# Optimization experiments

Hardware: AMD Instinct MI355X
Metric: run time of the kernel (lower is better)

The kernel has to match this reference:

```python
import jax, jax.numpy as jnp
import numpy as np

N_NODES = 100000
N_EDGES = 3200000
DIM = 64


def setup_inputs() -> dict:
    key = jax.random.key(0)
    k1, k2, k3, k4 = jax.random.split(key, 4)
    features = jax.random.normal(k1, (N_NODES, DIM), dtype=jnp.float32)
    attn_w = jax.random.normal(k2, (2 * DIM,), dtype=jnp.float32) / np.sqrt(2 * DIM)
    src = jax.random.randint(k3, (N_EDGES,), 0, N_NODES, dtype=jnp.int32)
    dst = jax.random.randint(k4, (N_EDGES,), 0, N_NODES, dtype=jnp.int32)
    return {"features": features, "attn_w": attn_w, "src": src, "dst": dst}


def reference(features, attn_w, src, dst):
    n = features.shape[0]
    d = features.shape[1]
    a_src, a_dst = attn_w[:d], attn_w[d:]
    # Edge attention: leaky_relu(Linear(concat(h_src, h_dst))) == leaky_relu(h_src@a_src + h_dst@a_dst)
    s_src = features @ a_src  # [N]
    s_dst = features @ a_dst  # [N]
    e = jax.nn.leaky_relu(s_src[src] + s_dst[dst], negative_slope=0.01)  # [E]
    # Segment softmax over incoming edges of each destination node
    emax = jax.ops.segment_max(e, dst, num_segments=n)  # [N], -inf for isolated nodes
    ee = jnp.exp(e - emax[dst])  # [E]
    denom = jax.ops.segment_sum(ee, dst, num_segments=n)  # [N]
    alpha = ee / denom[dst]  # [E]
    # Weighted neighbor aggregation (gather src feats, scatter-add into dst)
    h = jax.ops.segment_sum(alpha[:, None] * features[src], dst, num_segments=n)  # [N, D]
    return jax.nn.elu(h)
```

## Files before the change

kernel.cpp:

```cpp
#include <hip/hip_runtime.h>
#include <math.h>

#define DIM 64
#define SCAN_BLOCK 1024
#define NB1 1024
#define TPB2 1024
#define BUCKET_BITS 7
#define BUCKET_SZ 128
#define SRC_SHIFT 20
#define CAP 6144
#define CHUNK 12500
#define STAGE_SZ 12544

__device__ __forceinline__ float lrelu(float x) { return x > 0.f ? x : 0.01f * x; }
__device__ __forceinline__ float elu(float x)  { return x > 0.f ? x : expm1f(x); }

__global__ __launch_bounds__(TPB2)
void prep_scatter(const float* __restrict__ feat,
                  const float* __restrict__ attn_w,
                  float* __restrict__ s_src,
                  float* __restrict__ s_dst,
                  unsigned short* __restrict__ fbf,
                  int n_nodes,
                  const int* __restrict__ src,
                  const int* __restrict__ dst,
                  int* __restrict__ gcur,
                  int* __restrict__ bpk, int m, int nsb) {
    __shared__ int lh[NB1];
    __shared__ int bnd[NB1];
    __shared__ int cur[NB1];
    __shared__ int stage[STAGE_SZ];
    if (blockIdx.x < nsb) {
        int t = threadIdx.x;
        int lo = blockIdx.x * CHUNK;
        int hi = min(m, lo + CHUNK);
        int cc = hi - lo;
        int nbux = (n_nodes + BUCKET_SZ - 1) >> BUCKET_BITS;
        lh[t] = 0;
        __syncthreads();
        for (int i = lo + t; i < hi; i += TPB2)
            atomicAdd(&lh[dst[i] >> BUCKET_BITS], 1);
        __syncthreads();
        cur[t] = lh[t];
        __syncthreads();
        for (int off = 1; off < NB1; off <<= 1) {
            int u = (t >= off) ? cur[t - off] : 0;
            __syncthreads();
            cur[t] += u;
            __syncthreads();
        }
        int excl = cur[t] - lh[t];
        bnd[t] = excl;
        int c = lh[t];
        int gb = (c > 0) ? atomicAdd(&gcur[t], c) : 0;
        lh[t]  = gb;
        cur[t] = excl;
        __syncthreads();
        for (int i = lo + t; i < hi; i += TPB2) {
            int d = dst[i];
            int b = d >> BUCKET_BITS;
            int p = atomicAdd(&cur[b], 1);
            stage[p] = src[i] | ((d & (BUCKET_SZ - 1)) << SRC_SHIFT);
        }
        __syncthreads();
        for (int j = t; j < cc; j += TPB2) {
            int lo2 = 0, hi2 = nbux - 1;
            while (lo2 < hi2) {
                int mid = (lo2 + hi2 + 1) >> 1;
                if (bnd[mid] <= j) lo2 = mid; else hi2 = mid - 1;
            }
            int pos = lh[lo2] + (j - bnd[lo2]);
            if (pos < CAP)
                bpk[(size_t)lo2 * CAP + pos] = stage[j];
        }
        return;
    }
    int gid  = (blockIdx.x - nsb) * blockDim.x + threadIdx.x;
    int node = gid >> 4;
    int lane = gid & 15;
    if (node >= n_nodes) return;
    const float4 f  = *reinterpret_cast<const float4*>(feat + (size_t)node * DIM + lane * 4);
    const float4 as = *reinterpret_cast<const float4*>(attn_w + lane * 4);
    const float4 ad = *reinterpret_cast<const float4*>(attn_w + DIM + lane * 4);
    float ps = f.x * as.x + f.y * as.y + f.z * as.z + f.w * as.w;
    float pd = f.x * ad.x + f.y * ad.y + f.z * ad.z + f.w * ad.w;
    uint b0 = __float_as_uint(f.x), b1 = __float_as_uint(f.y);
    uint b2 = __float_as_uint(f.z), b3 = __float_as_uint(f.w);
    ushort4 h;
    h.x = (unsigned short)((b0 + 0x7FFFu + ((b0 >> 16) & 1u)) >> 16);
    h.y = (unsigned short)((b1 + 0x7FFFu + ((b1 >> 16) & 1u)) >> 16);
    h.z = (unsigned short)((b2 + 0x7FFFu + ((b2 >> 16) & 1u)) >> 16);
    h.w = (unsigned short)((b3 + 0x7FFFu + ((b3 >> 16) & 1u)) >> 16);
    *reinterpret_cast<ushort4*>(fbf + (size_t)node * DIM + lane * 4) = h;
    for (int off = 8; off >= 1; off >>= 1) {
        ps += __shfl_xor(ps, off, 16);
        pd += __shfl_xor(pd, off, 16);
    }
    if (lane == 0) {
        s_src[node] = ps;
        s_dst[node] = pd;
    }
}

__device__ __forceinline__ void bf16x8_acc(uint4 q, float w,
                                           float& a0, float& a1, float& a2, float& a3,
                                           float& a4, float& a5, float& a6, float& a7) {
    a0 += w * __uint_as_float(q.x << 16);
    a1 += w * __uint_as_float(q.x & 0xffff0000u);
    a2 += w * __uint_as_float(q.y << 16);
    a3 += w * __uint_as_float(q.y & 0xffff0000u);
    a4 += w * __uint_as_float(q.z << 16);
    a5 += w * __uint_as_float(q.z & 0xffff0000u);
    a6 += w * __uint_as_float(q.w << 16);
    a7 += w * __uint_as_float(q.w & 0xffff0000u);
}

__global__ __launch_bounds__(512)
void sort_aggregate(const int* __restrict__ bpk,
                    const int* __restrict__ gcur,
                    const float* __restrict__ s_src,
                    const float* __restrict__ s_dst,
                    const unsigned short* __restrict__ fbf,
                    float* __restrict__ out,
                    int n) {
    __shared__ float sdd[BUCKET_SZ];
    __shared__ int   hist[BUCKET_SZ];
    __shared__ int   offsl[BUCKET_SZ];
    __shared__ int   cur[BUCKET_SZ];
    __shared__ int   sA[BUCKET_SZ];
    __shared__ int   sB[BUCKET_SZ];
    __shared__ int   esrc_l[CAP];
    __shared__ float w_l[CAP];
    int b = blockIdx.x, t = threadIdx.x;
    int base = b * BUCKET_SZ;
    int cnt = min(gcur[b], CAP);
    const int*  bp  = bpk + (size_t)b * CAP;
    const uint4* bp4 = reinterpret_cast<const uint4*>(bp);
    int cnt4 = cnt >> 2;
    if (t < BUCKET_SZ) {
        hist[t] = 0;
        int nd = base + t;
        sdd[t] = (nd < n) ? s_dst[nd] : 0.f;
    }
    __syncthreads();
    for (int e = t; e < cnt4; e += 512) {
        uint4 v = bp4[e];
        atomicAdd(&hist[(v.x >> SRC_SHIFT) & (BUCKET_SZ - 1)], 1);
        atomicAdd(&hist[(v.y >> SRC_SHIFT) & (BUCKET_SZ - 1)], 1);
        atomicAdd(&hist[(v.z >> SRC_SHIFT) & (BUCKET_SZ - 1)], 1);
        atomicAdd(&hist[(v.w >> SRC_SHIFT) & (BUCKET_SZ - 1)], 1);
    }
    for (int e = (cnt4 << 2) + t; e < cnt; e += 512)
        atomicAdd(&hist[(bp[e] >> SRC_SHIFT) & (BUCKET_SZ - 1)], 1);
    __syncthreads();
    if (t < BUCKET_SZ) sA[t] = hist[t];
    __syncthreads();
    int* pin = sA; int* pout = sB;
    for (int off = 1; off < BUCKET_SZ; off <<= 1) {
        if (t < BUCKET_SZ) pout[t] = (t >= off) ? pin[t] + pin[t - off] : pin[t];
        __syncthreads();
        int* tmpp = pin; pin = pout; pout = tmpp;
    }
    if (t < BUCKET_SZ) {
        int excl = pin[t] - hist[t];
        offsl[t] = excl;
        cur[t] = excl;
    }
    __syncthreads();
    for (int e = t; e < cnt4; e += 512) {
        uint4 v = bp4[e];
        int sv0 = v.x & ((1 << SRC_SHIFT) - 1), dl0 = (v.x >> SRC_SHIFT) & (BUCKET_SZ - 1);
        int sv1 = v.y & ((1 << SRC_SHIFT) - 1), dl1 = (v.y >> SRC_SHIFT) & (BUCKET_SZ - 1);
        int sv2 = v.z & ((1 << SRC_SHIFT) - 1), dl2 = (v.z >> SRC_SHIFT) & (BUCKET_SZ - 1);
        int sv3 = v.w & ((1 << SRC_SHIFT) - 1), dl3 = (v.w >> SRC_SHIFT) & (BUCKET_SZ - 1);
        float w0 = __expf(lrelu(s_src[sv0] + sdd[dl0]));
        float w1 = __expf(lrelu(s_src[sv1] + sdd[dl1]));
        float w2 = __expf(lrelu(s_src[sv2] + sdd[dl2]));
        float w3 = __expf(lrelu(s_src[sv3] + sdd[dl3]));
        int p0 = atomicAdd(&cur[dl0], 1); esrc_l[p0] = sv0; w_l[p0] = w0;
        int p1 = atomicAdd(&cur[dl1], 1); esrc_l[p1] = sv1; w_l[p1] = w1;
        int p2 = atomicAdd(&cur[dl2], 1); esrc_l[p2] = sv2; w_l[p2] = w2;
        int p3 = atomicAdd(&cur[dl3], 1); esrc_l[p3] = sv3; w_l[p3] = w3;
    }
    for (int e = (cnt4 << 2) + t; e < cnt; e += 512) {
        int pk = bp[e];
        int sv = pk & ((1 << SRC_SHIFT) - 1);
        int dl = (pk >> SRC_SHIFT) & (BUCKET_SZ - 1);
        float w = __expf(lrelu(s_src[sv] + sdd[dl]));
        int p = atomicAdd(&cur[dl], 1);
        esrc_l[p] = sv;
        w_l[p] = w;
    }
    __syncthreads();
    int l8 = t & 7, grp = t >> 3;
    const uint4* fv4 = reinterpret_cast<const uint4*>(fbf);
    for (int node = grp; node < BUCKET_SZ; node += 64) {
        int st = offsl[node];
        int en = st + hist[node];
        float a0 = 0.f, a1 = 0.f, a2 = 0.f, a3 = 0.f;
        float a4 = 0.f, a5 = 0.f, a6 = 0.f, a7 = 0.f;
        float wsum = 0.f;
        int e = st;
        for (; e + 4 <= en; e += 4) {
            int   s0 = esrc_l[e],     s1 = esrc_l[e + 1];
            int   s2 = esrc_l[e + 2], s3 = esrc_l[e + 3];
            float w0 = w_l[e],        w1 = w_l[e + 1];
            float w2 = w_l[e + 2],    w3 = w_l[e + 3];
            uint4 q0 = fv4[(size_t)s0 * 8 + l8];
            uint4 q1 = fv4[(size_t)s1 * 8 + l8];
            uint4 q2 = fv4[(size_t)s2 * 8 + l8];
            uint4 q3 = fv4[(size_t)s3 * 8 + l8];
            wsum += (w0 + w1) + (w2 + w3);
            bf16x8_acc(q0, w0, a0, a1, a2, a3, a4, a5, a6, a7);
            bf16x8_acc(q1, w1, a0, a1, a2, a3, a4, a5, a6, a7);
            bf16x8_acc(q2, w2, a0, a1, a2, a3, a4, a5, a6, a7);
            bf16x8_acc(q3, w3, a0, a1, a2, a3, a4, a5, a6, a7);
        }
        for (; e < en; e++) {
            int   s0 = esrc_l[e];
            float w0 = w_l[e];
            uint4 q0 = fv4[(size_t)s0 * 8 + l8];
            wsum += w0;
            bf16x8_acc(q0, w0, a0, a1, a2, a3, a4, a5, a6, a7);
        }
        int nd = base + node;
        if (nd < n) {
            float inv = (en > st) ? 1.f / wsum : 0.f;
            float4 o1, o2;
            o1.x = elu(a0 * inv); o1.y = elu(a1 * inv);
            o1.z = elu(a2 * inv); o1.w = elu(a3 * inv);
            o2.x = elu(a4 * inv); o2.y = elu(a5 * inv);
            o2.z = elu(a6 * inv); o2.w = elu(a7 * inv);
            float4* orow = reinterpret_cast<float4*>(out + (size_t)nd * DIM + l8 * 8);
            orow[0] = o1;
            orow[1] = o2;
        }
    }
}

__global__ void compute_scores(const float* __restrict__ feat,
                               const float* __restrict__ attn_w,
                               float* __restrict__ s_src,
                               float* __restrict__ s_dst,
                               int n_nodes) {
    int gid  = blockIdx.x * blockDim.x + threadIdx.x;
    int node = gid >> 4;
    int lane = gid & 15;
    if (node >= n_nodes) return;
    const float4 f  = *reinterpret_cast<const float4*>(feat + (size_t)node * DIM + lane * 4);
    const float4 as = *reinterpret_cast<const float4*>(attn_w + lane * 4);
    const float4 ad = *reinterpret_cast<const float4*>(attn_w + DIM + lane * 4);
    float ps = f.x * as.x + f.y * as.y + f.z * as.z + f.w * as.w;
    float pd = f.x * ad.x + f.y * ad.y + f.z * ad.z + f.w * ad.w;
    for (int off = 8; off >= 1; off >>= 1) {
        ps += __shfl_xor(ps, off, 16);
        pd += __shfl_xor(pd, off, 16);
    }
    if (lane == 0) { s_src[node] = ps; s_dst[node] = pd; }
}

__global__ void scan_level1(const int* __restrict__ in, int* __restrict__ out,
                            int* __restrict__ bsum, int n) {
    __shared__ int tmp[SCAN_BLOCK];
    int t = threadIdx.x;
    int g = blockIdx.x * SCAN_BLOCK + t;
    int v = (g < n) ? in[g] : 0;
    tmp[t] = v;
    __syncthreads();
    for (int off = 1; off < SCAN_BLOCK; off <<= 1) {
        int u = (t >= off) ? tmp[t - off] : 0;
        __syncthreads();
        tmp[t] += u;
        __syncthreads();
    }
    if (g < n) out[g] = tmp[t] - v;
    if (t == SCAN_BLOCK - 1) bsum[blockIdx.x] = tmp[t];
}

__global__ void scan_level2(int* __restrict__ bsum, int nb) {
    __shared__ int tmp[SCAN_BLOCK];
    int t = threadIdx.x;
    int v = (t < nb) ? bsum[t] : 0;
    tmp[t] = v;
    __syncthreads();
    for (int off = 1; off < SCAN_BLOCK; off <<= 1) {
        int u = (t >= off) ? tmp[t - off] : 0;
        __syncthreads();
        tmp[t] += u;
        __syncthreads();
    }
    if (t < nb) bsum[t] = tmp[t] - v;
}

__global__ void scan_level3(int* __restrict__ out, const int* __restrict__ bsum,
                            int n) {
    int g = blockIdx.x * SCAN_BLOCK + threadIdx.x;
    if (g < n) out[g] += bsum[blockIdx.x];
}

__global__ void degree_rank(const int* __restrict__ dst, int* __restrict__ deg,
                            int* __restrict__ rank, int m) {
    int i = blockIdx.x * blockDim.x + threadIdx.x;
    if (i >= m) return;
    rank[i] = atomicAdd(&deg[dst[i]], 1);
}

__global__ void scatter_src(const int* __restrict__ src, const int* __restrict__ dst,
                            const int* __restrict__ rank, const int* __restrict__ offs,
                            int* __restrict__ esrc, int m) {
    int i = blockIdx.x * blockDim.x + threadIdx.x;
    if (i >= m) return;
    esrc[offs[dst[i]] + rank[i]] = src[i];
}

__global__ void aggregate_f32(const int* __restrict__ esrc,
                              const int* __restrict__ offs,
                              const int* __restrict__ deg,
                              const float* __restrict__ s_src,
                              const float* __restrict__ s_dst,
                              const float* __restrict__ feat,
                              float* __restrict__ out, int n) {
    int gid  = blockIdx.x * blockDim.x + threadIdx.x;
    int node = gid >> 4;
    int lane = gid & 15;
    if (node >= n) return;
    int start = offs[node];
    int cnt   = deg[node];
    float sdd = s_dst[node];
    const float4* fv = reinterpret_cast<const float4*>(feat);
    float4 acc = {0.f, 0.f, 0.f, 0.f};
    float wsum = 0.f;
    for (int e = 0; e < cnt; e++) {
        int s0 = esrc[start + e];
        float w0 = __expf(lrelu(s_src[s0] + sdd));
        float4 f0 = fv[s0 * 16 + lane];
        wsum += w0;
        acc.x += w0 * f0.x; acc.y += w0 * f0.y;
        acc.z += w0 * f0.z; acc.w += w0 * f0.w;
    }
    float inv = (cnt > 0) ? 1.f / wsum : 0.f;
    float4 o;
    o.x = elu(acc.x * inv); o.y = elu(acc.y * inv);
    o.z = elu(acc.z * inv); o.w = elu(acc.w * inv);
    reinterpret_cast<float4*>(out)[node * 16 + lane] = o;
}

extern "C" void kernel_launch(void* const* d_in, const int* in_sizes, int n_in,
                              void* d_out, int out_size, void* d_ws, size_t ws_size,
                              hipStream_t stream) {
    const float* feat   = (const float*)d_in[0];
    const float* attn_w = (const float*)d_in[1];
    const int*   src    = (const int*)d_in[2];
    const int*   dst    = (const int*)d_in[3];

    const int n = in_sizes[0] / DIM;
    const int m = in_sizes[2];

    float* out = (float*)d_out;

    const int nbux = (n + BUCKET_SZ - 1) >> BUCKET_BITS;

    float* s_src = (float*)d_ws;
    float* s_dst = s_src + n;
    unsigned short* fbf = (unsigned short*)(s_dst + n);
    int*   gcur  = (int*)(fbf + (size_t)n * DIM);
    int*   bpk   = gcur + NB1;
    size_t need  = ((size_t)(2 + DIM / 2) * n + NB1 + (size_t)nbux * CAP)
                   * sizeof(int);

    if (ws_size >= need && nbux <= NB1) {
        hipMemsetAsync(gcur, 0, (size_t)NB1 * sizeof(int), stream);

        int nsb = (m + CHUNK - 1) / CHUNK;
        int PB  = (n * 16 + TPB2 - 1) / TPB2;
        prep_scatter<<<nsb + PB, TPB2, 0, stream>>>(
            feat, attn_w, s_src, s_dst, fbf, n, src, dst, gcur, bpk, m, nsb);

        sort_aggregate<<<nbux, 512, 0, stream>>>(
            bpk, gcur, s_src, s_dst, fbf, out, n);
    } else {
        int* deg2  = (int*)(s_dst + n);
        int* offs2 = deg2 + n;
        int* bsum2 = offs2 + n;
        int* rank  = bsum2 + SCAN_BLOCK;
        int* esr2  = rank + m;
        int threads = n * 16;
        compute_scores<<<(threads + 255) / 256, 256, 0, stream>>>(
            feat, attn_w, s_src, s_dst, n);
        hipMemsetAsync(deg2, 0, (size_t)n * sizeof(int), stream);
        degree_rank<<<(m + 255) / 256, 256, 0, stream>>>(dst, deg2, rank, m);
        int nb2 = (n + SCAN_BLOCK - 1) / SCAN_BLOCK;
        scan_level1<<<nb2, SCAN_BLOCK, 0, stream>>>(deg2, offs2, bsum2, n);
        scan_level2<<<1, SCAN_BLOCK, 0, stream>>>(bsum2, nb2);
        scan_level3<<<nb2, SCAN_BLOCK, 0, stream>>>(offs2, bsum2, n);
        scatter_src<<<(m + 255) / 256, 256, 0, stream>>>(src, dst, rank, offs2, esr2, m);
        aggregate_f32<<<(threads + 255) / 256, 256, 0, stream>>>(
            esr2, offs2, deg2, s_src, s_dst, feat, out, n);
    }
}
```

Baseline: 192.6 us.

## Split each 128-node bucket across two 64-node blocks and replace binary search

The aggregation kernel now runs two 256-thread blocks per 128-node bucket. Each block reads the whole bucket list but keeps only the edges whose destination falls in its half, which gives more, smaller blocks and less shared memory per block for better occupancy. The cost is that every bucket list is read twice. In the scatter phase, the per-element binary search over bucket boundaries is replaced by a span lookup table (one entry per 16 staged elements) followed by a short linear walk. A new CAP2 limit silently truncates any half-bucket with more edges than it allows.

```diff
diff --git a/kernel.cpp b/kernel.cpp
--- a/kernel.cpp
+++ b/kernel.cpp
@@ -7,10 +7,13 @@
 #define TPB2 1024
 #define BUCKET_BITS 7
 #define BUCKET_SZ 128
+#define FB_SZ 64
 #define SRC_SHIFT 20
 #define CAP 6144
+#define CAP2 2560
 #define CHUNK 12500
 #define STAGE_SZ 12544
+#define NSPAN 784
 
 __device__ __forceinline__ float lrelu(float x) { return x > 0.f ? x : 0.01f * x; }
 __device__ __forceinline__ float elu(float x)  { return x > 0.f ? x : expm1f(x); }
@@ -29,6 +32,7 @@
     __shared__ int lh[NB1];
     __shared__ int bnd[NB1];
     __shared__ int cur[NB1];
+    __shared__ int span_b[NSPAN];
     __shared__ int stage[STAGE_SZ];
     if (blockIdx.x < nsb) {
         int t = threadIdx.x;
@@ -56,6 +60,11 @@
         lh[t]  = gb;
         cur[t] = excl;
         __syncthreads();
+        if (t < nbux) {
+            int s0 = (bnd[t] + 15) >> 4;
+            int s1 = (bnd[t + 1] + 15) >> 4;
+            for (int s = s0; s < s1; ++s) span_b[s] = t;
+        }
         for (int i = lo + t; i < hi; i += TPB2) {
             int d = dst[i];
             int b = d >> BUCKET_BITS;
@@ -64,14 +73,11 @@
         }
         __syncthreads();
         for (int j = t; j < cc; j += TPB2) {
-            int lo2 = 0, hi2 = nbux - 1;
-            while (lo2 < hi2) {
-                int mid = (lo2 + hi2 + 1) >> 1;
-                if (bnd[mid] <= j) lo2 = mid; else hi2 = mid - 1;
-            }
-            int pos = lh[lo2] + (j - bnd[lo2]);
+            int bkt = span_b[j >> 4];
+            while (bnd[bkt + 1] <= j) ++bkt;
+            int pos = lh[bkt] + (j - bnd[bkt]);
             if (pos < CAP)
-                bpk[(size_t)lo2 * CAP + pos] = stage[j];
+                bpk[(size_t)bkt * CAP + pos] = stage[j];
         }
         return;
     }
@@ -115,88 +121,79 @@
     a7 += w * __uint_as_float(q.w & 0xffff0000u);
 }
 
-__global__ __launch_bounds__(512)
-void sort_aggregate(const int* __restrict__ bpk,
-                    const int* __restrict__ gcur,
-                    const float* __restrict__ s_src,
-                    const float* __restrict__ s_dst,
-                    const unsigned short* __restrict__ fbf,
-                    float* __restrict__ out,
-                    int n) {
-    __shared__ float sdd[BUCKET_SZ];
-    __shared__ int   hist[BUCKET_SZ];
-    __shared__ int   offsl[BUCKET_SZ];
-    __shared__ int   cur[BUCKET_SZ];
-    __shared__ int   sA[BUCKET_SZ];
-    __shared__ int   sB[BUCKET_SZ];
-    __shared__ int   esrc_l[CAP];
-    __shared__ float w_l[CAP];
-    int b = blockIdx.x, t = threadIdx.x;
-    int base = b * BUCKET_SZ;
-    int cnt = min(gcur[b], CAP);
-    const int*  bp  = bpk + (size_t)b * CAP;
+__global__ __launch_bounds__(256)
+void sort_aggregate64(const int* __restrict__ bpk,
+                      const int* __restrict__ gcur,
+                      const float* __restrict__ s_src,
+                      const float* __restrict__ s_dst,
+                      const unsigned short* __restrict__ fbf,
+                      float* __restrict__ out,
+                      int n) {
+    __shared__ float sdd[FB_SZ];
+    __shared__ int   hist[FB_SZ];
+    __shared__ int   offsl[FB_SZ];
+    __shared__ int   cur[FB_SZ];
+    __shared__ int   sA[FB_SZ];
+    __shared__ int   sB[FB_SZ];
+    __shared__ int   esrc_l[CAP2];
+    __shared__ float w_l[CAP2];
+    int f = blockIdx.x, t = threadIdx.x;
+    int cb = f >> 1;
+    int hb = (f & 1) << 6;
+    int base = f * FB_SZ;
+    int cnt = min(gcur[cb], CAP);
+    const int*  bp  = bpk + (size_t)cb * CAP;
     const uint4* bp4 = reinterpret_cast<const uint4*>(bp);
     int cnt4 = cnt >> 2;
-    if (t < BUCKET_SZ) {
+    if (t < FB_SZ) {
         hist[t] = 0;
         int nd = base + t;
         sdd[t] = (nd < n) ? s_dst[nd] : 0.f;
     }
     __syncthreads();
-    for (int e = t; e < cnt4; e += 512) {
+#define HPROC(pk) { int dl7_ = ((pk) >> SRC_SHIFT) & 127; \
+    if ((dl7_ & 64) == hb) atomicAdd(&hist[dl7_ & 63], 1); }
+    for (int e = t; e < cnt4; e += 256) {
         uint4 v = bp4[e];
-        atomicAdd(&hist[(v.x >> SRC_SHIFT) & (BUCKET_SZ - 1)], 1);
-        atomicAdd(&hist[(v.y >> SRC_SHIFT) & (BUCKET_SZ - 1)], 1);
-        atomicAdd(&hist[(v.z >> SRC_SHIFT) & (BUCKET_SZ - 1)], 1);
-        atomicAdd(&hist[(v.w >> SRC_SHIFT) & (BUCKET_SZ - 1)], 1);
-    }
-    for (int e = (cnt4 << 2) + t; e < cnt; e += 512)
-        atomicAdd(&hist[(bp[e] >> SRC_SHIFT) & (BUCKET_SZ - 1)], 1);
-    __syncthreads();
-    if (t < BUCKET_SZ) sA[t] = hist[t];
-    __syncthreads();
-    int* pin = sA; int* pout = sB;
-    for (int off = 1; off < BUCKET_SZ; off <<= 1) {
-        if (t < BUCKET_SZ) pout[t] = (t >= off) ? pin[t] + pin[t - off] : pin[t];
-        __syncthreads();
-        int* tmpp = pin; pin = pout; pout = tmpp;
-    }
-    if (t < BUCKET_SZ) {
-        int excl = pin[t] - hist[t];
-        offsl[t] = excl;
-        cur[t] = excl;
-    }
-    __syncthreads();
-    for (int e = t; e < cnt4; e += 512) {
+        HPROC((int)v.x) HPROC((int)v.y) HPROC((int)v.z) HPROC((int)v.w)
+    }
+    for (int e = (cnt4 << 2) + t; e < cnt; e += 256)
+        HPROC(bp[e])
+    __syncthreads();
+    if (t < FB_SZ) sA[t] = hist[t];
+    __syncthreads();
+    {
+        int* pin = sA; int* pout = sB;
+        for (int off = 1; off < FB_SZ; off <<= 1) {
+            if (t < FB_SZ) pout[t] = (t >= off) ? pin[t] + pin[t - off] : pin[t];
+            __syncthreads();
+            int* tmpp = pin; pin = pout; pout = tmpp;
+        }
+        if (t < FB_SZ) {
+            int excl = min(pin[t] - hist[t], CAP2);
+            offsl[t] = excl;
+            cur[t] = excl;
+        }
+    }
+    __syncthreads();
+#define SPROC(pk) { int dl7_ = ((pk) >> SRC_SHIFT) & 127; \
+    if ((dl7_ & 64) == hb) { \
+        int sv_ = (pk) & ((1 << SRC_SHIFT) - 1); \
+        float w_ = __expf(lrelu(s_src[sv_] + sdd[dl7_ & 63])); \
+        int p_ = atomicAdd(&cur[dl7_ & 63], 1); \
+        if (p_ < CAP2) { esrc_l[p_] = sv_; w_l[p_] = w_; } } }
+    for (int e = t; e < cnt4; e += 256) {
         uint4 v = bp4[e];
-        int sv0 = v.x & ((1 << SRC_SHIFT) - 1), dl0 = (v.x >> SRC_SHIFT) & (BUCKET_SZ - 1);
-        int sv1 = v.y & ((1 << SRC_SHIFT) - 1), dl1 = (v.y >> SRC_SHIFT) & (BUCKET_SZ - 1);
-        int sv2 = v.z & ((1 << SRC_SHIFT) - 1), dl2 = (v.z >> SRC_SHIFT) & (BUCKET_SZ - 1);
-        int sv3 = v.w & ((1 << SRC_SHIFT) - 1), dl3 = (v.w >> SRC_SHIFT) & (BUCKET_SZ - 1);
-        float w0 = __expf(lrelu(s_src[sv0] + sdd[dl0]));
-        float w1 = __expf(lrelu(s_src[sv1] + sdd[dl1]));
-        float w2 = __expf(lrelu(s_src[sv2] + sdd[dl2]));
-        float w3 = __expf(lrelu(s_src[sv3] + sdd[dl3]));
-        int p0 = atomicAdd(&cur[dl0], 1); esrc_l[p0] = sv0; w_l[p0] = w0;
-        int p1 = atomicAdd(&cur[dl1], 1); esrc_l[p1] = sv1; w_l[p1] = w1;
-        int p2 = atomicAdd(&cur[dl2], 1); esrc_l[p2] = sv2; w_l[p2] = w2;
-        int p3 = atomicAdd(&cur[dl3], 1); esrc_l[p3] = sv3; w_l[p3] = w3;
-    }
-    for (int e = (cnt4 << 2) + t; e < cnt; e += 512) {
-        int pk = bp[e];
-        int sv = pk & ((1 << SRC_SHIFT) - 1);
-        int dl = (pk >> SRC_SHIFT) & (BUCKET_SZ - 1);
-        float w = __expf(lrelu(s_src[sv] + sdd[dl]));
-        int p = atomicAdd(&cur[dl], 1);
-        esrc_l[p] = sv;
-        w_l[p] = w;
-    }
+        SPROC((int)v.x) SPROC((int)v.y) SPROC((int)v.z) SPROC((int)v.w)
+    }
+    for (int e = (cnt4 << 2) + t; e < cnt; e += 256)
+        SPROC(bp[e])
     __syncthreads();
     int l8 = t & 7, grp = t >> 3;
     const uint4* fv4 = reinterpret_cast<const uint4*>(fbf);
-    for (int node = grp; node < BUCKET_SZ; node += 64) {
+    for (int node = grp; node < FB_SZ; node += 32) {
         int st = offsl[node];
-        int en = st + hist[node];
+        int en = min(st + hist[node], CAP2);
         float a0 = 0.f, a1 = 0.f, a2 = 0.f, a3 = 0.f;
         float a4 = 0.f, a5 = 0.f, a6 = 0.f, a7 = 0.f;
         float wsum = 0.f;
@@ -236,6 +233,8 @@
             orow[1] = o2;
         }
     }
+#undef HPROC
+#undef SPROC
 }
 
 __global__ void compute_scores(const float* __restrict__ feat,
@@ -359,6 +358,7 @@
     float* out = (float*)d_out;
 
     const int nbux = (n + BUCKET_SZ - 1) >> BUCKET_BITS;
+    const int nfb  = (n + FB_SZ - 1) / FB_SZ;
 
     float* s_src = (float*)d_ws;
     float* s_dst = s_src + n;
@@ -376,7 +376,7 @@
         prep_scatter<<<nsb + PB, TPB2, 0, stream>>>(
             feat, attn_w, s_src, s_dst, fbf, n, src, dst, gcur, bpk, m, nsb);
 
-        sort_aggregate<<<nbux, 512, 0, stream>>>(
+        sort_aggregate64<<<nfb, 256, 0, stream>>>(
             bpk, gcur, s_src, s_dst, fbf, out, n);
     } else {
         int* deg2  = (int*)(s_dst + n);
```

Result: faster. 187.8 us (-2.5%).
